# Performance work log

Hardware: AMD Instinct MI355X
Metric: run time of the kernel (lower is better)

Reference implementation:

```python
import jax, jax.numpy as jnp
import numpy as np

HEAD_DIM = 64
NUM_HEADS = 16
ROPE_BASE = 10000.0


def _rope_cos_sin(seq_len, head_dim, dtype):
    inv_freq = 1.0 / (ROPE_BASE ** (jnp.arange(0, head_dim, 2, dtype=jnp.float32) / head_dim))
    t = jnp.arange(seq_len, dtype=jnp.float32)
    freqs = jnp.outer(t, inv_freq)                      # [S, D/2]
    emb = jnp.concatenate([freqs, freqs], axis=-1)      # [S, D]
    return jnp.cos(emb).astype(dtype), jnp.sin(emb).astype(dtype)


def _rotate_half(x):
    x1, x2 = jnp.split(x, 2, axis=-1)
    return jnp.concatenate([-x2, x1], axis=-1)


def setup_inputs() -> dict:
    key = jax.random.key(0)
    ks = jax.random.split(key, 5)
    B, S, H = 2, 2048, 1024
    x = jax.random.normal(ks[0], (B, S, H), dtype=jnp.float32)
    attention_mask = jnp.ones((B, S), dtype=jnp.float32)
    scale = 0.02
    Wq = jax.random.normal(ks[1], (H, H), dtype=jnp.float32) * scale
    Wk = jax.random.normal(ks[2], (H, H), dtype=jnp.float32) * scale
    Wv = jax.random.normal(ks[3], (H, H), dtype=jnp.float32) * scale
    Wo = jax.random.normal(ks[4], (H, H), dtype=jnp.float32) * scale
    return {"x": x, "attention_mask": attention_mask, "Wq": Wq, "Wk": Wk, "Wv": Wv, "Wo": Wo}


def reference(x, attention_mask, Wq, Wk, Wv, Wo):
    B, S, H = x.shape
    nh, hd = NUM_HEADS, HEAD_DIM
    scale = hd ** -0.5

    # nn.Linear semantics: y = x @ W^T  (W is [out, in])
    q = jnp.einsum('bsh,oh->bso', x, Wq).reshape(B, S, nh, hd).transpose(0, 2, 1, 3)
    k = jnp.einsum('bsh,oh->bso', x, Wk).reshape(B, S, nh, hd).transpose(0, 2, 1, 3)
    v = jnp.einsum('bsh,oh->bso', x, Wv).reshape(B, S, nh, hd).transpose(0, 2, 1, 3)

    cos, sin = _rope_cos_sin(S, hd, x.dtype)            # [S, hd]
    cos = cos[None, None, :, :]
    sin = sin[None, None, :, :]
    q = q * cos + _rotate_half(q) * sin
    k = k * cos + _rotate_half(k) * sin

    attn = jnp.einsum('bhqd,bhkd->bhqk', q, k) * scale  # [B, nh, S, S]
    mask = (1.0 - attention_mask.astype(x.dtype))[:, None, None, :] * jnp.finfo(x.dtype).min
    attn = attn + mask
    attn = jax.nn.softmax(attn, axis=-1)
    out = jnp.einsum('bhqk,bhkd->bhqd', attn, v)        # [B, nh, S, hd]
    out = out.transpose(0, 2, 1, 3).reshape(B, S, nh * hd)
    return jnp.einsum('bso,ho->bsh', out, Wo)
```

## Files before the change

kernel.cpp:

```cpp
#include <hip/hip_runtime.h>
#include <math.h>

#define BB 2
#define SS 2048
#define HH 1024
#define NH 16
#define HD 64
#define MM (BB*SS)

typedef __attribute__((ext_vector_type(8))) _Float16 f16x8;
typedef __attribute__((ext_vector_type(2))) __fp16 hf16x2;
typedef __attribute__((ext_vector_type(4))) float f32x4;

#define QSCALE 0.18033688011112042f

__device__ __forceinline__ unsigned short f2h(float f) {
    union { _Float16 h; unsigned short u; } c;
    c.h = (_Float16)f;
    return c.u;
}

__device__ __forceinline__ unsigned int pkh(float a, float b) {
    union { hf16x2 h; unsigned int u; } c;
    c.h = __builtin_amdgcn_cvt_pkrtz(a, b);
    return c.u;
}

__device__ __forceinline__ void gld16(const void* g, void* s) {
    __builtin_amdgcn_global_load_lds(
        (const __attribute__((address_space(1))) void*)g,
        (__attribute__((address_space(3))) void*)s, 16, 0, 0);
}

__global__ __launch_bounds__(256) void prep(
    const float* __restrict__ x, const float* __restrict__ mask,
    const float* __restrict__ Wq, const float* __restrict__ Wk,
    const float* __restrict__ Wv, const float* __restrict__ Wo,
    unsigned short* __restrict__ xf, unsigned short* __restrict__ wf,
    float* __restrict__ ctab, float* __restrict__ stab, float* __restrict__ mt,
    unsigned int* __restrict__ mflag)
{
    int gtid = blockIdx.x * 256 + threadIdx.x;
    if (gtid < SS * 32) {
        int s = gtid >> 5, i = gtid & 31;
        double invf = pow(10000.0, -(double)i / 32.0);
        double a = (double)s * invf;
        ctab[gtid] = (float)cos(a);
        stab[gtid] = (float)sin(a);
    }
    if (gtid < BB * SS) {
        float mv = mask[gtid];
        mt[gtid] = (1.0f - mv) * (-1.0e38f);
        unsigned long long bal = __ballot(mv == 1.0f);
        if ((threadIdx.x & 63) == 0)
            mflag[gtid >> 6] = (bal == ~0ull) ? 1u : 0u;
    }
    for (int it = gtid; it < 2097152; it += 524288) {
        float4 v; unsigned short* d; size_t off;
        if (it < 1048576) {
            off = (size_t)it * 4;
            v = *(const float4*)(x + off);
            d = xf;
        } else {
            off = (size_t)(it - 1048576) * 4;
            int row = (int)(off >> 10);
            const float* W = row < 1024 ? Wq : row < 2048 ? Wk : row < 3072 ? Wv : Wo;
            v = *(const float4*)(W + (((size_t)(row & 1023)) << 10) + (off & 1023));
            d = wf;
        }
        *(ushort4*)(d + off) = make_ushort4(f2h(v.x), f2h(v.y), f2h(v.z), f2h(v.w));
    }
}

template<int MODE>
__global__ __launch_bounds__(256, 3) void gemm3(
    const unsigned short* __restrict__ Axf,
    const unsigned short* __restrict__ Wf,
    const float* __restrict__ ctab, const float* __restrict__ stab,
    unsigned short* __restrict__ qo, unsigned short* __restrict__ ko,
    unsigned short* __restrict__ vo, float* __restrict__ fout)
{
    __shared__ __align__(16) short lsA[2][128*32];
    __shared__ __align__(16) short lsB[2][128*32];

    const int t = threadIdx.x;
    const int m0 = blockIdx.x * 128;
    const int brow0 = (MODE == 0 ? 0 : 3072) + blockIdx.y * 128;
    const int lane = t & 63, wv = t >> 6;
    const int wm = (wv >> 1) * 64, wn = (wv & 1) * 64;
    const int fr = lane & 15, fg = lane >> 4;

    const int srow = t >> 2, pc = t & 3;
    const int scx = (pc ^ ((srow >> 1) & 3)) * 8;
    const int lo  = srow * 32 + pc * 8;
    const size_t gA0 = (size_t)(m0 + srow) * HH + scx;
    const size_t gA1 = (size_t)(m0 + 64 + srow) * HH + scx;
    const size_t gB0 = (size_t)(brow0 + srow) * HH + scx;
    const size_t gB1 = (size_t)(brow0 + 64 + srow) * HH + scx;

    f32x4 acc[4][4] = {};

#define STAGE(sel, kk) do { \
        gld16(Axf + gA0 + (kk), &lsA[sel][lo]);            \
        gld16(Wf  + gB0 + (kk), &lsB[sel][lo]);            \
        gld16(Axf + gA1 + (kk), &lsA[sel][lo + 64*32]);    \
        gld16(Wf  + gB1 + (kk), &lsB[sel][lo + 64*32]);    \
    } while (0)

    STAGE(0, 0);
    __syncthreads();

    int cur = 0;
    for (int k0 = 0; k0 < HH; k0 += 32) {
        if (k0 + 32 < HH) STAGE(cur ^ 1, k0 + 32);

        f16x8 ah[4], bh[4];
        const int swz = (fg ^ ((fr >> 1) & 3)) * 8;
        #pragma unroll
        for (int mi = 0; mi < 4; ++mi)
            ah[mi] = *(const f16x8*)&lsA[cur][(wm + 16*mi + fr)*32 + swz];
        #pragma unroll
        for (int ni = 0; ni < 4; ++ni)
            bh[ni] = *(const f16x8*)&lsB[cur][(wn + 16*ni + fr)*32 + swz];

        __builtin_amdgcn_s_setprio(1);
        #pragma unroll
        for (int mi = 0; mi < 4; ++mi)
            #pragma unroll
            for (int ni = 0; ni < 4; ++ni)
                acc[mi][ni] = __builtin_amdgcn_mfma_f32_16x16x32_f16(ah[mi], bh[ni], acc[mi][ni], 0, 0, 0);
        __builtin_amdgcn_s_setprio(0);
        __syncthreads();
        cur ^= 1;
    }
#undef STAGE

    if (MODE == 0) {
        const int mat = brow0 >> 10;
        const int obase = (brow0 & 1023) + wn;
        const int h = obase >> 6;
        #pragma unroll
        for (int mi = 0; mi < 4; ++mi)
            #pragma unroll
            for (int rr = 0; rr < 4; ++rr) {
                int m = m0 + wm + 16*mi + 4*fg + rr;
                int b = m >> 11, s = m & (SS - 1);
                float v[4];
                #pragma unroll
                for (int ni = 0; ni < 4; ++ni) v[ni] = acc[mi][ni][rr];
                if (mat < 2) {
                    #pragma unroll
                    for (int ni = 0; ni < 2; ++ni) {
                        int i = 16*ni + fr;
                        float c = ctab[s*32 + i], sn = stab[s*32 + i];
                        float v1 = v[ni], v2 = v[ni + 2];
                        v[ni]     = v1*c - v2*sn;
                        v[ni + 2] = v2*c + v1*sn;
                    }
                }
                if (mat == 0) {
                    #pragma unroll
                    for (int ni = 0; ni < 4; ++ni) v[ni] *= QSCALE;
                }
                size_t base = ((size_t)(b*NH + h) * SS + s) * HD;
                #pragma unroll
                for (int ni = 0; ni < 4; ++ni) {
                    int d = 16*ni + fr;
                    unsigned short hb = f2h(v[ni]);
                    if (mat == 0)      qo[base + d] = hb;
                    else if (mat == 1) ko[base + (d ^ ((s & 7) << 3))] = hb;
                    else {
                        size_t va = ((size_t)(b*NH + h) * HD + d) * SS
                                  + (s & ~63) + ((s & 63) ^ ((d & 7) << 3));
                        vo[va] = hb;
                    }
                }
            }
    } else {
        const int n0 = blockIdx.y * 128 + wn;
        #pragma unroll
        for (int mi = 0; mi < 4; ++mi)
            #pragma unroll
            for (int rr = 0; rr < 4; ++rr) {
                int m = m0 + wm + 16*mi + 4*fg + rr;
                #pragma unroll
                for (int ni = 0; ni < 4; ++ni)
                    fout[(size_t)m * HH + n0 + 16*ni + fr] = acc[mi][ni][rr];
            }
    }
}

__global__ __launch_bounds__(512, 2) void attn(
    const unsigned short* __restrict__ qg, const unsigned short* __restrict__ kg,
    const unsigned short* __restrict__ vtg, const float* __restrict__ mt,
    const unsigned int* __restrict__ mfl, unsigned short* __restrict__ cf)
{
    __shared__ __align__(16) short Ks[2][64*64];
    __shared__ __align__(16) short Vs[2][64*64];
    __shared__ __align__(16) short Ps[128*64];

    const int t = threadIdx.x, lane = t & 63, wv = t >> 6;
    const int fr = lane & 15, fg = lane >> 4, frx = fr & 7;
    const int flat = blockIdx.x;
    const int bh = (flat & 7) + ((flat >> 7) << 3);
    const int q0 = ((flat >> 3) & 15) * 128;
    const int b = bh >> 4, h = bh & 15;

    const unsigned short* kgb = kg  + (size_t)bh*SS*HD;
    const unsigned short* vgb = vtg + (size_t)bh*HD*SS;
    const float* mtb = mt + (size_t)b*SS;
    const unsigned int* mfb = mfl + b*32;

    f16x8 qa[2];
    #pragma unroll
    for (int kc = 0; kc < 2; ++kc)
        qa[kc] = *(const f16x8*)&qg[((size_t)bh*SS + q0 + 16*wv + fr)*HD + kc*32 + fg*8];

    f16x8 onev;
    #pragma unroll
    for (int i = 0; i < 8; ++i) onev[i] = (_Float16)1.0f;

    f32x4 o[4] = {};
    f32x4 oS = {};
    const int pbase = (wv*16 + fr) * 64;
    const int hs = (fr >> 3) * 4;

    const int srow = t >> 3, sg = t & 7;

    gld16(kgb + (size_t)srow*HD + sg*8, &Ks[0][srow*64 + sg*8]);
    gld16(vgb + (size_t)srow*SS + sg*8, &Vs[0][srow*64 + sg*8]);
    __syncthreads();

    int cur = 0;
    for (int kt = 0; kt < SS/64; ++kt) {
        const int k0 = kt * 64;
        if (kt + 1 < SS/64) {
            const int kn = k0 + 64;
            gld16(kgb + (size_t)(kn+srow)*HD + sg*8, &Ks[cur^1][srow*64 + sg*8]);
            gld16(vgb + (size_t)srow*SS + kn + sg*8, &Vs[cur^1][srow*64 + sg*8]);
        }
        const int fl = __builtin_amdgcn_readfirstlane(mfb[kt]);

        f32x4 sc[4] = {};
        __builtin_amdgcn_s_setprio(1);
        #pragma unroll
        for (int kc = 0; kc < 2; ++kc) {
            #pragma unroll
            for (int nf = 0; nf < 4; ++nf) {
                int gr = (4*kc + fg) ^ frx;
                f16x8 kb = *(const f16x8*)&Ks[cur][(16*nf + fr)*64 + gr*8];
                sc[nf] = __builtin_amdgcn_mfma_f32_16x16x32_f16(kb, qa[kc], sc[nf], 0, 0, 0);
            }
        }
        __builtin_amdgcn_s_setprio(0);

        if (fl) {
            #pragma unroll
            for (int nf = 0; nf < 4; ++nf) {
                float p0 = __builtin_amdgcn_exp2f(sc[nf][0]);
                float p1 = __builtin_amdgcn_exp2f(sc[nf][1]);
                float p2 = __builtin_amdgcn_exp2f(sc[nf][2]);
                float p3 = __builtin_amdgcn_exp2f(sc[nf][3]);
                uint2 w; w.x = pkh(p0, p1); w.y = pkh(p2, p3);
                *(uint2*)&Ps[pbase + (((2*nf + (fg >> 1)) ^ frx) * 8) + (4*(fg & 1) ^ hs)] = w;
            }
        } else {
            #pragma unroll
            for (int nf = 0; nf < 4; ++nf) {
                float4 m4 = *(const float4*)&mtb[k0 + 16*nf + 4*fg];
                float p0 = __builtin_amdgcn_exp2f(sc[nf][0] + m4.x);
                float p1 = __builtin_amdgcn_exp2f(sc[nf][1] + m4.y);
                float p2 = __builtin_amdgcn_exp2f(sc[nf][2] + m4.z);
                float p3 = __builtin_amdgcn_exp2f(sc[nf][3] + m4.w);
                uint2 w; w.x = pkh(p0, p1); w.y = pkh(p2, p3);
                *(uint2*)&Ps[pbase + (((2*nf + (fg >> 1)) ^ frx) * 8) + (4*(fg & 1) ^ hs)] = w;
            }
        }

        __builtin_amdgcn_s_setprio(1);
        #pragma unroll
        for (int kc = 0; kc < 2; ++kc) {
            int pg = pbase + (((4*kc + fg) ^ frx) * 8);
            union { f16x8 v; uint2 q[2]; } pu;
            pu.q[0] = *(const uint2*)&Ps[pg + hs];
            pu.q[1] = *(const uint2*)&Ps[pg + (hs ^ 4)];
            f16x8 pa = pu.v;
            #pragma unroll
            for (int df = 0; df < 4; ++df) {
                f16x8 vb = *(const f16x8*)&Vs[cur][(16*df + fr)*64 + ((4*kc + fg) ^ frx)*8];
                o[df] = __builtin_amdgcn_mfma_f32_16x16x32_f16(vb, pa, o[df], 0, 0, 0);
            }
            oS = __builtin_amdgcn_mfma_f32_16x16x32_f16(onev, pa, oS, 0, 0, 0);
        }
        __builtin_amdgcn_s_setprio(0);
        __syncthreads();
        cur ^= 1;
    }

    float inv = 1.0f / oS[0];
    size_t base = ((size_t)b*SS + q0 + 16*wv + fr)*HH + h*HD;
    #pragma unroll
    for (int df = 0; df < 4; ++df) {
        uint2 w;
        w.x = pkh(o[df][0]*inv, o[df][1]*inv);
        w.y = pkh(o[df][2]*inv, o[df][3]*inv);
        *(uint2*)&cf[base + 16*df + 4*fg] = w;
    }
}

extern "C" void kernel_launch(void* const* d_in, const int* in_sizes, int n_in,
                              void* d_out, int out_size, void* d_ws, size_t ws_size,
                              hipStream_t stream) {
    const float* x    = (const float*)d_in[0];
    const float* mask = (const float*)d_in[1];
    const float* Wq   = (const float*)d_in[2];
    const float* Wk   = (const float*)d_in[3];
    const float* Wv   = (const float*)d_in[4];
    const float* Wo   = (const float*)d_in[5];
    float* out = (float*)d_out;

    const size_t T = (size_t)MM * HH;
    unsigned short* xf = (unsigned short*)d_ws;
    unsigned short* wf = xf + T;
    unsigned short* qt = wf + T;
    unsigned short* kt = qt + T;
    unsigned short* vt = kt + T;
    float* ctab = (float*)(vt + T);
    float* stab = ctab + SS*32;
    float* mt   = stab + SS*32;
    unsigned int* mfg = (unsigned int*)(mt + BB*SS);
    unsigned short* cf = xf;

    prep<<<2048, 256, 0, stream>>>(x, mask, Wq, Wk, Wv, Wo, xf, wf, ctab, stab, mt, mfg);
    gemm3<0><<<dim3(MM/128, 3*HH/128), 256, 0, stream>>>(xf, wf, ctab, stab,
                                                         qt, kt, vt, nullptr);
    attn<<<512, 512, 0, stream>>>(qt, kt, vt, mt, mfg, cf);
    gemm3<1><<<dim3(MM/128, HH/128), 256, 0, stream>>>(cf, wf, nullptr, nullptr,
                                                       nullptr, nullptr, nullptr, out);
}
```

Before: 113.4 us.

## Give each attention wave two 16-row query tiles to reuse K/V fragments

The attention kernel now runs 4 waves of 256 threads per block instead of 8, and each wave handles 32 query rows as two 16-row sub-tiles. Each K and V fragment read from LDS feeds two MFMAs, which halves LDS reads per MFMA. Staging loads are split into two gld16 calls per thread so the same 64x64 tiles are filled with fewer threads. The cost is double the accumulator and score registers per wave, which may lower occupancy (launch bounds now ask for 3 blocks per CU), and fewer waves to hide latency.

After: 113.8 us. About the same (+0.4%).

```diff
diff --git a/kernel.cpp b/kernel.cpp
--- a/kernel.cpp
+++ b/kernel.cpp
@@ -190,7 +190,7 @@
     }
 }
 
-__global__ __launch_bounds__(512, 2) void attn(
+__global__ __launch_bounds__(256, 3) void attn(
     const unsigned short* __restrict__ qg, const unsigned short* __restrict__ kg,
     const unsigned short* __restrict__ vtg, const float* __restrict__ mt,
     const unsigned int* __restrict__ mfl, unsigned short* __restrict__ cf)
@@ -211,24 +211,30 @@
     const float* mtb = mt + (size_t)b*SS;
     const unsigned int* mfb = mfl + b*32;
 
-    f16x8 qa[2];
+    f16x8 qa[2][2];
     #pragma unroll
-    for (int kc = 0; kc < 2; ++kc)
-        qa[kc] = *(const f16x8*)&qg[((size_t)bh*SS + q0 + 16*wv + fr)*HD + kc*32 + fg*8];
+    for (int mi = 0; mi < 2; ++mi)
+        #pragma unroll
+        for (int kc = 0; kc < 2; ++kc)
+            qa[mi][kc] = *(const f16x8*)&qg[((size_t)bh*SS + q0 + 32*wv + 16*mi + fr)*HD + kc*32 + fg*8];
 
     f16x8 onev;
     #pragma unroll
     for (int i = 0; i < 8; ++i) onev[i] = (_Float16)1.0f;
 
-    f32x4 o[4] = {};
-    f32x4 oS = {};
-    const int pbase = (wv*16 + fr) * 64;
+    f32x4 o[2][4] = {};
+    f32x4 oS[2] = {};
+    int pb[2];
+    #pragma unroll
+    for (int mi = 0; mi < 2; ++mi) pb[mi] = (32*wv + 16*mi + fr) * 64;
     const int hs = (fr >> 3) * 4;
 
     const int srow = t >> 3, sg = t & 7;
 
-    gld16(kgb + (size_t)srow*HD + sg*8, &Ks[0][srow*64 + sg*8]);
-    gld16(vgb + (size_t)srow*SS + sg*8, &Vs[0][srow*64 + sg*8]);
+    gld16(kgb + (size_t)srow*HD + sg*8,      &Ks[0][srow*64 + sg*8]);
+    gld16(kgb + (size_t)(32+srow)*HD + sg*8, &Ks[0][(32+srow)*64 + sg*8]);
+    gld16(vgb + (size_t)srow*SS + sg*8,      &Vs[0][srow*64 + sg*8]);
+    gld16(vgb + (size_t)(32+srow)*SS + sg*8, &Vs[0][(32+srow)*64 + sg*8]);
     __syncthreads();
 
     int cur = 0;
@@ -236,12 +242,14 @@
         const int k0 = kt * 64;
         if (kt + 1 < SS/64) {
             const int kn = k0 + 64;
-            gld16(kgb + (size_t)(kn+srow)*HD + sg*8, &Ks[cur^1][srow*64 + sg*8]);
-            gld16(vgb + (size_t)srow*SS + kn + sg*8, &Vs[cur^1][srow*64 + sg*8]);
+            gld16(kgb + (size_t)(kn+srow)*HD + sg*8,      &Ks[cur^1][srow*64 + sg*8]);
+            gld16(kgb + (size_t)(kn+32+srow)*HD + sg*8,   &Ks[cur^1][(32+srow)*64 + sg*8]);
+            gld16(vgb + (size_t)srow*SS + kn + sg*8,      &Vs[cur^1][srow*64 + sg*8]);
+            gld16(vgb + (size_t)(32+srow)*SS + kn + sg*8, &Vs[cur^1][(32+srow)*64 + sg*8]);
         }
         const int fl = __builtin_amdgcn_readfirstlane(mfb[kt]);
 
-        f32x4 sc[4] = {};
+        f32x4 sc[2][4] = {};
         __builtin_amdgcn_s_setprio(1);
         #pragma unroll
         for (int kc = 0; kc < 2; ++kc) {
@@ -249,62 +257,80 @@
             for (int nf = 0; nf < 4; ++nf) {
                 int gr = (4*kc + fg) ^ frx;
                 f16x8 kb = *(const f16x8*)&Ks[cur][(16*nf + fr)*64 + gr*8];
-                sc[nf] = __builtin_amdgcn_mfma_f32_16x16x32_f16(kb, qa[kc], sc[nf], 0, 0, 0);
+                #pragma unroll
+                for (int mi = 0; mi < 2; ++mi)
+                    sc[mi][nf] = __builtin_amdgcn_mfma_f32_16x16x32_f16(kb, qa[mi][kc], sc[mi][nf], 0, 0, 0);
             }
         }
         __builtin_amdgcn_s_setprio(0);
 
         if (fl) {
             #pragma unroll
-            for (int nf = 0; nf < 4; ++nf) {
-                float p0 = __builtin_amdgcn_exp2f(sc[nf][0]);
-                float p1 = __builtin_amdgcn_exp2f(sc[nf][1]);
-                float p2 = __builtin_amdgcn_exp2f(sc[nf][2]);
-                float p3 = __builtin_amdgcn_exp2f(sc[nf][3]);
-                uint2 w; w.x = pkh(p0, p1); w.y = pkh(p2, p3);
-                *(uint2*)&Ps[pbase + (((2*nf + (fg >> 1)) ^ frx) * 8) + (4*(fg & 1) ^ hs)] = w;
-            }
+            for (int mi = 0; mi < 2; ++mi)
+                #pragma unroll
+                for (int nf = 0; nf < 4; ++nf) {
+                    float p0 = __builtin_amdgcn_exp2f(sc[mi][nf][0]);
+                    float p1 = __builtin_amdgcn_exp2f(sc[mi][nf][1]);
+                    float p2 = __builtin_amdgcn_exp2f(sc[mi][nf][2]);
+                    float p3 = __builtin_amdgcn_exp2f(sc[mi][nf][3]);
+                    uint2 w; w.x = pkh(p0, p1); w.y = pkh(p2, p3);
+                    *(uint2*)&Ps[pb[mi] + (((2*nf + (fg >> 1)) ^ frx) * 8) + (4*(fg & 1) ^ hs)] = w;
+                }
         } else {
             #pragma unroll
-            for (int nf = 0; nf < 4; ++nf) {
-                float4 m4 = *(const float4*)&mtb[k0 + 16*nf + 4*fg];
-                float p0 = __builtin_amdgcn_exp2f(sc[nf][0] + m4.x);
-                float p1 = __builtin_amdgcn_exp2f(sc[nf][1] + m4.y);
-                float p2 = __builtin_amdgcn_exp2f(sc[nf][2] + m4.z);
-                float p3 = __builtin_amdgcn_exp2f(sc[nf][3] + m4.w);
-                uint2 w; w.x = pkh(p0, p1); w.y = pkh(p2, p3);
-                *(uint2*)&Ps[pbase + (((2*nf + (fg >> 1)) ^ frx) * 8) + (4*(fg & 1) ^ hs)] = w;
-            }
+            for (int mi = 0; mi < 2; ++mi)
+                #pragma unroll
+                for (int nf = 0; nf < 4; ++nf) {
+                    float4 m4 = *(const float4*)&mtb[k0 + 16*nf + 4*fg];
+                    float p0 = __builtin_amdgcn_exp2f(sc[mi][nf][0] + m4.x);
+                    float p1 = __builtin_amdgcn_exp2f(sc[mi][nf][1] + m4.y);
+                    float p2 = __builtin_amdgcn_exp2f(sc[mi][nf][2] + m4.z);
+                    float p3 = __builtin_amdgcn_exp2f(sc[mi][nf][3] + m4.w);
+                    uint2 w; w.x = pkh(p0, p1); w.y = pkh(p2, p3);
+                    *(uint2*)&Ps[pb[mi] + (((2*nf + (fg >> 1)) ^ frx) * 8) + (4*(fg & 1) ^ hs)] = w;
+                }
         }
 
         __builtin_amdgcn_s_setprio(1);
         #pragma unroll
         for (int kc = 0; kc < 2; ++kc) {
-            int pg = pbase + (((4*kc + fg) ^ frx) * 8);
-            union { f16x8 v; uint2 q[2]; } pu;
-            pu.q[0] = *(const uint2*)&Ps[pg + hs];
-            pu.q[1] = *(const uint2*)&Ps[pg + (hs ^ 4)];
-            f16x8 pa = pu.v;
+            const int gr = (4*kc + fg) ^ frx;
+            f16x8 pa[2];
+            #pragma unroll
+            for (int mi = 0; mi < 2; ++mi) {
+                int pg = pb[mi] + gr*8;
+                union { f16x8 v; uint2 q[2]; } pu;
+                pu.q[0] = *(const uint2*)&Ps[pg + hs];
+                pu.q[1] = *(const uint2*)&Ps[pg + (hs ^ 4)];
+                pa[mi] = pu.v;
+            }
             #pragma unroll
             for (int df = 0; df < 4; ++df) {
-                f16x8 vb = *(const f16x8*)&Vs[cur][(16*df + fr)*64 + ((4*kc + fg) ^ frx)*8];
-                o[df] = __builtin_amdgcn_mfma_f32_16x16x32_f16(vb, pa, o[df], 0, 0, 0);
-            }
-            oS = __builtin_amdgcn_mfma_f32_16x16x32_f16(onev, pa, oS, 0, 0, 0);
+                f16x8 vb = *(const f16x8*)&Vs[cur][(16*df + fr)*64 + gr*8];
+                #pragma unroll
+                for (int mi = 0; mi < 2; ++mi)
+                    o[mi][df] = __builtin_amdgcn_mfma_f32_16x16x32_f16(vb, pa[mi], o[mi][df], 0, 0, 0);
+            }
+            #pragma unroll
+            for (int mi = 0; mi < 2; ++mi)
+                oS[mi] = __builtin_amdgcn_mfma_f32_16x16x32_f16(onev, pa[mi], oS[mi], 0, 0, 0);
         }
         __builtin_amdgcn_s_setprio(0);
         __syncthreads();
         cur ^= 1;
     }
 
-    float inv = 1.0f / oS[0];
-    size_t base = ((size_t)b*SS + q0 + 16*wv + fr)*HH + h*HD;
     #pragma unroll
-    for (int df = 0; df < 4; ++df) {
-        uint2 w;
-        w.x = pkh(o[df][0]*inv, o[df][1]*inv);
-        w.y = pkh(o[df][2]*inv, o[df][3]*inv);
-        *(uint2*)&cf[base + 16*df + 4*fg] = w;
+    for (int mi = 0; mi < 2; ++mi) {
+        float inv = 1.0f / oS[mi][0];
+        size_t base = ((size_t)b*SS + q0 + 32*wv + 16*mi + fr)*HH + h*HD;
+        #pragma unroll
+        for (int df = 0; df < 4; ++df) {
+            uint2 w;
+            w.x = pkh(o[mi][df][0]*inv, o[mi][df][1]*inv);
+            w.y = pkh(o[mi][df][2]*inv, o[mi][df][3]*inv);
+            *(uint2*)&cf[base + 16*df + 4*fg] = w;
+        }
     }
 }
 
@@ -334,7 +360,7 @@
     prep<<<2048, 256, 0, stream>>>(x, mask, Wq, Wk, Wv, Wo, xf, wf, ctab, stab, mt, mfg);
     gemm3<0><<<dim3(MM/128, 3*HH/128), 256, 0, stream>>>(xf, wf, ctab, stab,
                                                          qt, kt, vt, nullptr);
-    attn<<<512, 512, 0, stream>>>(qt, kt, vt, mt, mfg, cf);
+    attn<<<512, 256, 0, stream>>>(qt, kt, vt, mt, mfg, cf);
     gemm3<1><<<dim3(MM/128, HH/128), 256, 0, stream>>>(cf, wf, nullptr, nullptr,
                                                        nullptr, nullptr, nullptr, out);
 }
```
